# Optimization experiments

Hardware: AMD Instinct MI355X
Metric: run time of the kernel (lower is better)

## Reference

```python
import jax, jax.numpy as jnp
import numpy as np

N_NODES = 100000
N_EDGES = 3200000
IN_F, HID, N_CLS = 1433, 16, 7


def setup_inputs() -> dict:
    key = jax.random.key(0)
    ks = jax.random.split(key, 6)
    return {
        "x": jax.random.normal(ks[0], (N_NODES, IN_F), dtype=jnp.float32),
        "W1": jax.random.normal(ks[1], (IN_F, HID), dtype=jnp.float32) * 0.02,
        "b1": jax.random.normal(ks[2], (HID,), dtype=jnp.float32) * 0.02,
        "W2": jax.random.normal(ks[3], (HID, N_CLS), dtype=jnp.float32) * 0.1,
        "b2": jax.random.normal(ks[4], (N_CLS,), dtype=jnp.float32) * 0.1,
        "edge_index": jax.random.randint(ks[5], (2, N_EDGES), 0, N_NODES, dtype=jnp.int64),
    }


def _gcn_layer(h, W, b, row, col, n_nodes):
    # dense linear
    h = h @ W + b
    # symmetric degree normalization (self-loops already appended)
    deg = jax.ops.segment_sum(jnp.ones_like(col, dtype=h.dtype), col, num_segments=n_nodes)
    dinv = deg ** -0.5
    norm = dinv[row] * dinv[col]  # [E]
    # gather-scale-scatter message passing (aggr='add', source row -> target col)
    msgs = norm[:, None] * h[row]  # [E, F_out]
    return jax.ops.segment_sum(msgs, col, num_segments=n_nodes)


def reference(x, W1, b1, W2, b2, edge_index):
    n = x.shape[0]
    self_loops = jnp.broadcast_to(jnp.arange(n, dtype=edge_index.dtype)[None, :], (2, n))
    ei = jnp.concatenate([edge_index, self_loops], axis=1)
    row, col = ei[0], ei[1]
    h = jax.nn.relu(_gcn_layer(x, W1, b1, row, col, n))
    h = jax.nn.relu(_gcn_layer(h, W2, b2, row, col, n))
    return jax.nn.log_softmax(h, axis=1)
```

## Files before the change

### kernel.cpp

```cpp
#include <hip/hip_runtime.h>
#include <math.h>

constexpr int K_IN  = 1433;
constexpr int HID   = 16;
constexpr int NCLS  = 7;
constexpr int BLK   = 256;
constexpr int NB    = 256;
constexpr int NBLKA = 1024;

__device__ inline float4 wave_reduce4(float4 v) {
#pragma unroll
  for (int off = 32; off > 0; off >>= 1) {
    v.x += __shfl_xor(v.x, off);
    v.y += __shfl_xor(v.y, off);
    v.z += __shfl_xor(v.z, off);
    v.w += __shfl_xor(v.w, off);
  }
  return v;
}

__device__ inline int block_excl_scan256(int v, int* wsum) {
  const int lane = threadIdx.x & 63, wid = threadIdx.x >> 6;
  int s = v;
#pragma unroll
  for (int off = 1; off < 64; off <<= 1) {
    int t = __shfl_up(s, off);
    if (lane >= off) s += t;
  }
  if (lane == 63) wsum[wid] = s;
  __syncthreads();
  int woff = 0;
#pragma unroll
  for (int k = 0; k < 4; ++k) woff += (k < wid) ? wsum[k] : 0;
  return woff + s - v;
}


__global__ __launch_bounds__(256) void k_histA(const int* __restrict__ col,
                                               int* __restrict__ gHist, int nE) {
  __shared__ int h[NB];
  h[threadIdx.x] = 0;
  __syncthreads();
  const int ch = (nE + NBLKA - 1) / NBLKA;
  const int e0 = blockIdx.x * ch;
  const int e1 = min(e0 + ch, nE);
  for (int e = e0 + threadIdx.x; e < e1; e += 256) atomicAdd(&h[col[e] >> 9], 1);
  __syncthreads();
  gHist[threadIdx.x * NBLKA + blockIdx.x] = h[threadIdx.x];
}

__global__ __launch_bounds__(256) void k_scanA(int* __restrict__ gHist,
                                               int* __restrict__ bTot) {
  __shared__ int wsum[4];
  const int b = blockIdx.x, t = threadIdx.x;
  int4* p = (int4*)(gHist + (size_t)b * NBLKA);
  int4 c = p[t];
  const int tsum = c.x + c.y + c.z + c.w;
  const int base = block_excl_scan256(tsum, wsum);
  int4 o; o.x = base; o.y = base + c.x; o.z = o.y + c.y; o.w = o.z + c.z;
  p[t] = o;
  if (t == 255) bTot[b] = base + tsum;
}

__global__ __launch_bounds__(256) void k_placeA(const int* __restrict__ row,
                                                const int* __restrict__ col,
                                                const int* __restrict__ gHist,
                                                const int* __restrict__ bTot,
                                                int* __restrict__ sorted, int nE) {
  __shared__ int cur[NB];
  __shared__ int wsum[4];
  const int t = threadIdx.x;
  const int excl = block_excl_scan256(bTot[t], wsum);
  cur[t] = excl + gHist[t * NBLKA + blockIdx.x];
  __syncthreads();
  const int ch = (nE + NBLKA - 1) / NBLKA;
  const int e0 = blockIdx.x * ch;
  const int e1 = min(e0 + ch, nE);
  for (int e = e0 + t; e < e1; e += 256) {
    const int c = col[e];
    const int p = atomicAdd(&cur[c >> 9], 1);
    sorted[p] = ((c & 511) << 17) | row[e];
  }
}

__global__ __launch_bounds__(256) void k_bucketB(const int* __restrict__ sorted,
                                                 const int* __restrict__ bTot,
                                                 int* __restrict__ cnt,
                                                 int* __restrict__ start,
                                                 float* __restrict__ dinv,
                                                 int* __restrict__ rows, int n) {
  __shared__ int h[512];
  __shared__ int ls[512];
  __shared__ int sBase[NB];
  __shared__ int wsum[4];
  const int b = blockIdx.x, t = threadIdx.x;
  const int lane = t & 63, wid = t >> 6;
  h[t] = 0; h[t + 256] = 0;
  sBase[t] = block_excl_scan256(bTot[t], wsum);
  __syncthreads();
  const int s0 = sBase[b];
  const int s1 = (b < 255) ? sBase[b + 1] : s0 + bTot[b];
  for (int e = s0 + t; e < s1; e += 256) atomicAdd(&h[(sorted[e] >> 17) & 511], 1);
  __syncthreads();
  const int c0 = h[2 * t], c1 = h[2 * t + 1];
  const int tsum = c0 + c1;
  int s = tsum;
#pragma unroll
  for (int off = 1; off < 64; off <<= 1) { int v = __shfl_up(s, off); if (lane >= off) s += v; }
  if (lane == 63) wsum[wid] = s;
  __syncthreads();
  int woff = 0;
#pragma unroll
  for (int k = 0; k < 4; ++k) woff += (k < wid) ? wsum[k] : 0;
  const int base = woff + s - tsum;
  ls[2 * t] = base;
  ls[2 * t + 1] = base + c0;
  const int gc0 = b * 512 + 2 * t;
  if (gc0 < n) {
    cnt[gc0] = c0; start[gc0] = s0 + base;
    dinv[gc0] = rsqrtf((float)(c0 + 1));
  }
  if (gc0 + 1 < n) {
    cnt[gc0 + 1] = c1; start[gc0 + 1] = s0 + base + c0;
    dinv[gc0 + 1] = rsqrtf((float)(c1 + 1));
  }
  __syncthreads();
  for (int e = s0 + t; e < s1; e += 256) {
    const int rc = sorted[e];
    const int p = atomicAdd(&ls[(rc >> 17) & 511], 1);
    rows[s0 + p] = rc & 0x1FFFF;
  }
}


__global__ __launch_bounds__(BLK) void k_gemm1(const float* __restrict__ x,
                                               const float* __restrict__ W1,
                                               const float* __restrict__ b1,
                                               const float* __restrict__ dinv,
                                               float* __restrict__ h1s, int n) {
  const int lane = threadIdx.x & 63;
  const int wave = threadIdx.x >> 6;
  const int r0 = blockIdx.x * 16 + wave * 4;
  bool vr[4];
  const float* xr[4];
#pragma unroll
  for (int j = 0; j < 4; ++j) {
    vr[j] = (r0 + j) < n;
    xr[j] = x + (size_t)(vr[j] ? r0 + j : 0) * K_IN;
  }
  float acc[4][HID] = {};

  constexpr int NSTEP = (K_IN + 63) / 64;
#pragma unroll 2
  for (int s = 0; s < NSTEP - 1; ++s) {
    const int k = s * 64 + lane;
    const float4* wp = (const float4*)(W1 + (size_t)k * HID);
    const float4 w0 = wp[0], w1 = wp[1], w2 = wp[2], w3 = wp[3];
    float xv[4];
#pragma unroll
    for (int j = 0; j < 4; ++j) xv[j] = vr[j] ? xr[j][k] : 0.0f;
#pragma unroll
    for (int j = 0; j < 4; ++j) {
      acc[j][0]  = fmaf(xv[j], w0.x, acc[j][0]);
      acc[j][1]  = fmaf(xv[j], w0.y, acc[j][1]);
      acc[j][2]  = fmaf(xv[j], w0.z, acc[j][2]);
      acc[j][3]  = fmaf(xv[j], w0.w, acc[j][3]);
      acc[j][4]  = fmaf(xv[j], w1.x, acc[j][4]);
      acc[j][5]  = fmaf(xv[j], w1.y, acc[j][5]);
      acc[j][6]  = fmaf(xv[j], w1.z, acc[j][6]);
      acc[j][7]  = fmaf(xv[j], w1.w, acc[j][7]);
      acc[j][8]  = fmaf(xv[j], w2.x, acc[j][8]);
      acc[j][9]  = fmaf(xv[j], w2.y, acc[j][9]);
      acc[j][10] = fmaf(xv[j], w2.z, acc[j][10]);
      acc[j][11] = fmaf(xv[j], w2.w, acc[j][11]);
      acc[j][12] = fmaf(xv[j], w3.x, acc[j][12]);
      acc[j][13] = fmaf(xv[j], w3.y, acc[j][13]);
      acc[j][14] = fmaf(xv[j], w3.z, acc[j][14]);
      acc[j][15] = fmaf(xv[j], w3.w, acc[j][15]);
    }
  }
  {
    const int k = (NSTEP - 1) * 64 + lane;
    if (k < K_IN) {
      const float4* wp = (const float4*)(W1 + (size_t)k * HID);
      const float4 ww[4] = {wp[0], wp[1], wp[2], wp[3]};
      float xv[4];
#pragma unroll
      for (int j = 0; j < 4; ++j) xv[j] = vr[j] ? xr[j][k] : 0.0f;
#pragma unroll
      for (int j = 0; j < 4; ++j)
#pragma unroll
        for (int f4 = 0; f4 < 4; ++f4) {
          acc[j][f4 * 4 + 0] = fmaf(xv[j], ww[f4].x, acc[j][f4 * 4 + 0]);
          acc[j][f4 * 4 + 1] = fmaf(xv[j], ww[f4].y, acc[j][f4 * 4 + 1]);
          acc[j][f4 * 4 + 2] = fmaf(xv[j], ww[f4].z, acc[j][f4 * 4 + 2]);
          acc[j][f4 * 4 + 3] = fmaf(xv[j], ww[f4].w, acc[j][f4 * 4 + 3]);
        }
    }
  }

  const float4* b14 = (const float4*)b1;
#pragma unroll
  for (int j = 0; j < 4; ++j) {
    float4 a[4];
#pragma unroll
    for (int f4 = 0; f4 < 4; ++f4)
      a[f4] = wave_reduce4(make_float4(acc[j][f4 * 4], acc[j][f4 * 4 + 1],
                                       acc[j][f4 * 4 + 2], acc[j][f4 * 4 + 3]));
    if (lane == 0 && vr[j]) {
      const int r = r0 + j;
      const float d = dinv[r];
      float4* o = (float4*)(h1s + (size_t)r * HID);
#pragma unroll
      for (int f4 = 0; f4 < 4; ++f4) {
        const float4 bb = b14[f4];
        o[f4] = make_float4(d * (a[f4].x + bb.x), d * (a[f4].y + bb.y),
                            d * (a[f4].z + bb.z), d * (a[f4].w + bb.w));
      }
    }
  }
}

__global__ __launch_bounds__(BLK) void k_gather1g2(const int* __restrict__ rows,
                                                   const int* __restrict__ start,
                                                   const int* __restrict__ cnt,
                                                   const float* __restrict__ dinv,
                                                   const float* __restrict__ h1s,
                                                   const float* __restrict__ W2,
                                                   const float* __restrict__ b2,
                                                   float* __restrict__ h2s, int n) {
  __shared__ float w2s[HID * NCLS];
  __shared__ float b2s[NCLS];
  if (threadIdx.x < HID * NCLS) w2s[threadIdx.x] = W2[threadIdx.x];
  if (threadIdx.x < NCLS) b2s[threadIdx.x] = b2[threadIdx.x];
  __syncthreads();
  const int node = blockIdx.x * 4 + (threadIdx.x >> 6);
  const int lane = threadIdx.x & 63;
  const int f = lane & 15;
  const int g = lane >> 4;
  if (node >= n) return;
  const float dc = dinv[node];
  float acc = (g == 0) ? h1s[(size_t)node * HID + f] : 0.0f;
  const int m = cnt[node];
  const int* bp = rows + start[node];
  int q = g;
  for (; q + 4 < m; q += 8) {
    const int r0 = bp[q], r1 = bp[q + 4];
    acc += h1s[(size_t)r0 * HID + f];
    acc += h1s[(size_t)r1 * HID + f];
  }
  if (q < m) acc += h1s[(size_t)bp[q] * HID + f];
  acc += __shfl_xor(acc, 16);
  acc += __shfl_xor(acc, 32);
  acc = fmaxf(dc * acc, 0.0f);
  float sj[NCLS];
#pragma unroll
  for (int j = 0; j < NCLS; ++j) sj[j] = acc * w2s[f * NCLS + j];
#pragma unroll
  for (int off = 1; off < 16; off <<= 1)
#pragma unroll
    for (int j = 0; j < NCLS; ++j) sj[j] += __shfl_xor(sj[j], off);
  if (g == 0 && f < NCLS) {
    float v = sj[0];
#pragma unroll
    for (int j = 1; j < NCLS; ++j) if (f == j) v = sj[j];
    h2s[(size_t)node * NCLS + f] = dc * (v + b2s[f]);
  }
}

__global__ __launch_bounds__(BLK) void k_gather2(const int* __restrict__ rows,
                                                 const int* __restrict__ start,
                                                 const int* __restrict__ cnt,
                                                 const float* __restrict__ dinv,
                                                 const float* __restrict__ h2s,
                                                 float* __restrict__ out, int n) {
  const int node = blockIdx.x * 4 + (threadIdx.x >> 6);
  const int lane = threadIdx.x & 63;
  const int f = lane & 7;
  const int g = lane >> 3;
  if (node >= n) return;
  const float dc = dinv[node];
  float acc = (g == 0) ? h2s[(size_t)node * NCLS + f] : 0.0f;
  const int m = cnt[node];
  const int* bp = rows + start[node];
  int q = g;
  for (; q + 8 < m; q += 16) {
    const int r0 = bp[q], r1 = bp[q + 8];
    acc += h2s[(size_t)r0 * NCLS + f];
    acc += h2s[(size_t)r1 * NCLS + f];
  }
  if (q < m) acc += h2s[(size_t)bp[q] * NCLS + f];
  acc += __shfl_xor(acc, 8);
  acc += __shfl_xor(acc, 16);
  acc += __shfl_xor(acc, 32);
  const bool act = f < NCLS;
  const float t = fmaxf(dc * acc, 0.0f);
  float tm = act ? t : -1e30f;
#pragma unroll
  for (int off = 1; off < 8; off <<= 1) tm = fmaxf(tm, __shfl_xor(tm, off, 8));
  float se = act ? __expf(t - tm) : 0.0f;
#pragma unroll
  for (int off = 1; off < 8; off <<= 1) se += __shfl_xor(se, off, 8);
  const float lse = tm + __logf(se);
  if (g == 0 && act) out[(size_t)node * NCLS + f] = t - lse;
}

extern "C" void kernel_launch(void* const* d_in, const int* in_sizes, int n_in,
                              void* d_out, int out_size, void* d_ws, size_t ws_size,
                              hipStream_t stream) {
  const float* x  = (const float*)d_in[0];
  const float* W1 = (const float*)d_in[1];
  const float* b1 = (const float*)d_in[2];
  const float* W2 = (const float*)d_in[3];
  const float* b2 = (const float*)d_in[4];
  const int*   ei = (const int*)d_in[5];

  const int n  = in_sizes[0] / K_IN;
  const int nE = in_sizes[5] / 2;
  const int* row = ei;
  const int* col = ei + nE;

  char* w = (char*)d_ws;
  size_t off = 0;
  auto alloc = [&](size_t elems) {
    void* p = w + off;
    off += ((elems * 4 + 15) & ~(size_t)15);
    return p;
  };
  int*   cnt    = (int*)alloc(n);
  int*   start  = (int*)alloc(n);
  float* dinv   = (float*)alloc(n);
  float* h1s    = (float*)alloc((size_t)n * HID);
  float* h2s    = (float*)alloc((size_t)n * NCLS + 16);
  int*   gHist  = (int*)alloc((size_t)NB * NBLKA);
  int*   bTot   = (int*)alloc(NB);
  int*   sorted = (int*)alloc(nE);
  int*   rows   = (int*)alloc(nE);

  const int gG1 = (n + 15) / 16;
  const int gWN = (n + 3) / 4;

  k_histA<<<NBLKA, 256, 0, stream>>>(col, gHist, nE);
  k_scanA<<<NB, 256, 0, stream>>>(gHist, bTot);
  k_placeA<<<NBLKA, 256, 0, stream>>>(row, col, gHist, bTot, sorted, nE);
  k_bucketB<<<NB, 256, 0, stream>>>(sorted, bTot, cnt, start, dinv, rows, n);

  k_gemm1<<<gG1, BLK, 0, stream>>>(x, W1, b1, dinv, h1s, n);
  k_gather1g2<<<gWN, BLK, 0, stream>>>(rows, start, cnt, dinv, h1s, W2, b2, h2s, n);

  k_gather2<<<gWN, BLK, 0, stream>>>(rows, start, cnt, dinv, h2s, (float*)d_out, n);
}
```

Baseline: 419.2 us.

## Overlap GEMM1 with edge-sorting kernels by splitting it across fused launches

The dense x@W1 GEMM no longer waits for the degree computation. It no longer scales by dinv and is split into three row segments. Each segment runs as extra blocks inside the histogram, placement and bucket kernels, so the memory-bound GEMM overlaps the sorting phases. The dinv scaling moves into the first gather, which now loads dinv for each source row. This adds random reads per edge, and the hardcoded segment sizes assume n=100000.

```diff
diff --git a/kernel.cpp b/kernel.cpp
--- a/kernel.cpp
+++ b/kernel.cpp
@@ -7,6 +7,9 @@
 constexpr int BLK   = 256;
 constexpr int NB    = 256;
 constexpr int NBLKA = 1024;
+constexpr int GSEG1 = 2083;
+constexpr int GSEG2 = 2083;
+constexpr int GSEG3 = 2084;
 
 __device__ inline float4 wave_reduce4(float4 v) {
 #pragma unroll
@@ -35,112 +38,14 @@
   return woff + s - v;
 }
 
-
-__global__ __launch_bounds__(256) void k_histA(const int* __restrict__ col,
-                                               int* __restrict__ gHist, int nE) {
-  __shared__ int h[NB];
-  h[threadIdx.x] = 0;
-  __syncthreads();
-  const int ch = (nE + NBLKA - 1) / NBLKA;
-  const int e0 = blockIdx.x * ch;
-  const int e1 = min(e0 + ch, nE);
-  for (int e = e0 + threadIdx.x; e < e1; e += 256) atomicAdd(&h[col[e] >> 9], 1);
-  __syncthreads();
-  gHist[threadIdx.x * NBLKA + blockIdx.x] = h[threadIdx.x];
-}
-
-__global__ __launch_bounds__(256) void k_scanA(int* __restrict__ gHist,
-                                               int* __restrict__ bTot) {
-  __shared__ int wsum[4];
-  const int b = blockIdx.x, t = threadIdx.x;
-  int4* p = (int4*)(gHist + (size_t)b * NBLKA);
-  int4 c = p[t];
-  const int tsum = c.x + c.y + c.z + c.w;
-  const int base = block_excl_scan256(tsum, wsum);
-  int4 o; o.x = base; o.y = base + c.x; o.z = o.y + c.y; o.w = o.z + c.z;
-  p[t] = o;
-  if (t == 255) bTot[b] = base + tsum;
-}
-
-__global__ __launch_bounds__(256) void k_placeA(const int* __restrict__ row,
-                                                const int* __restrict__ col,
-                                                const int* __restrict__ gHist,
-                                                const int* __restrict__ bTot,
-                                                int* __restrict__ sorted, int nE) {
-  __shared__ int cur[NB];
-  __shared__ int wsum[4];
-  const int t = threadIdx.x;
-  const int excl = block_excl_scan256(bTot[t], wsum);
-  cur[t] = excl + gHist[t * NBLKA + blockIdx.x];
-  __syncthreads();
-  const int ch = (nE + NBLKA - 1) / NBLKA;
-  const int e0 = blockIdx.x * ch;
-  const int e1 = min(e0 + ch, nE);
-  for (int e = e0 + t; e < e1; e += 256) {
-    const int c = col[e];
-    const int p = atomicAdd(&cur[c >> 9], 1);
-    sorted[p] = ((c & 511) << 17) | row[e];
-  }
-}
-
-__global__ __launch_bounds__(256) void k_bucketB(const int* __restrict__ sorted,
-                                                 const int* __restrict__ bTot,
-                                                 int* __restrict__ cnt,
-                                                 int* __restrict__ start,
-                                                 float* __restrict__ dinv,
-                                                 int* __restrict__ rows, int n) {
-  __shared__ int h[512];
-  __shared__ int ls[512];
-  __shared__ int sBase[NB];
-  __shared__ int wsum[4];
-  const int b = blockIdx.x, t = threadIdx.x;
-  const int lane = t & 63, wid = t >> 6;
-  h[t] = 0; h[t + 256] = 0;
-  sBase[t] = block_excl_scan256(bTot[t], wsum);
-  __syncthreads();
-  const int s0 = sBase[b];
-  const int s1 = (b < 255) ? sBase[b + 1] : s0 + bTot[b];
-  for (int e = s0 + t; e < s1; e += 256) atomicAdd(&h[(sorted[e] >> 17) & 511], 1);
-  __syncthreads();
-  const int c0 = h[2 * t], c1 = h[2 * t + 1];
-  const int tsum = c0 + c1;
-  int s = tsum;
-#pragma unroll
-  for (int off = 1; off < 64; off <<= 1) { int v = __shfl_up(s, off); if (lane >= off) s += v; }
-  if (lane == 63) wsum[wid] = s;
-  __syncthreads();
-  int woff = 0;
-#pragma unroll
-  for (int k = 0; k < 4; ++k) woff += (k < wid) ? wsum[k] : 0;
-  const int base = woff + s - tsum;
-  ls[2 * t] = base;
-  ls[2 * t + 1] = base + c0;
-  const int gc0 = b * 512 + 2 * t;
-  if (gc0 < n) {
-    cnt[gc0] = c0; start[gc0] = s0 + base;
-    dinv[gc0] = rsqrtf((float)(c0 + 1));
-  }
-  if (gc0 + 1 < n) {
-    cnt[gc0 + 1] = c1; start[gc0 + 1] = s0 + base + c0;
-    dinv[gc0 + 1] = rsqrtf((float)(c1 + 1));
-  }
-  __syncthreads();
-  for (int e = s0 + t; e < s1; e += 256) {
-    const int rc = sorted[e];
-    const int p = atomicAdd(&ls[(rc >> 17) & 511], 1);
-    rows[s0 + p] = rc & 0x1FFFF;
-  }
-}
-
-
-__global__ __launch_bounds__(BLK) void k_gemm1(const float* __restrict__ x,
-                                               const float* __restrict__ W1,
-                                               const float* __restrict__ b1,
-                                               const float* __restrict__ dinv,
-                                               float* __restrict__ h1s, int n) {
+__device__ __forceinline__ void gemm1_block(int gblk,
+                                            const float* __restrict__ x,
+                                            const float* __restrict__ W1,
+                                            const float* __restrict__ b1,
+                                            float* __restrict__ h1lin, int n) {
   const int lane = threadIdx.x & 63;
   const int wave = threadIdx.x >> 6;
-  const int r0 = blockIdx.x * 16 + wave * 4;
+  const int r0 = gblk * 16 + wave * 4;
   bool vr[4];
   const float* xr[4];
 #pragma unroll
@@ -209,15 +114,135 @@
                                        acc[j][f4 * 4 + 2], acc[j][f4 * 4 + 3]));
     if (lane == 0 && vr[j]) {
       const int r = r0 + j;
-      const float d = dinv[r];
-      float4* o = (float4*)(h1s + (size_t)r * HID);
+      float4* o = (float4*)(h1lin + (size_t)r * HID);
 #pragma unroll
       for (int f4 = 0; f4 < 4; ++f4) {
         const float4 bb = b14[f4];
-        o[f4] = make_float4(d * (a[f4].x + bb.x), d * (a[f4].y + bb.y),
-                            d * (a[f4].z + bb.z), d * (a[f4].w + bb.w));
+        o[f4] = make_float4(a[f4].x + bb.x, a[f4].y + bb.y,
+                            a[f4].z + bb.z, a[f4].w + bb.w);
       }
     }
+  }
+}
+
+__global__ __launch_bounds__(256) void k_fusedA(const int* __restrict__ col,
+                                                int* __restrict__ gHist, int nE,
+                                                const float* __restrict__ x,
+                                                const float* __restrict__ W1,
+                                                const float* __restrict__ b1,
+                                                float* __restrict__ h1lin, int n) {
+  __shared__ int h[NB];
+  if (blockIdx.x < NBLKA) {
+    const int b = blockIdx.x;
+    h[threadIdx.x] = 0;
+    __syncthreads();
+    const int ch = (nE + NBLKA - 1) / NBLKA;
+    const int e0 = b * ch;
+    const int e1 = min(e0 + ch, nE);
+    for (int e = e0 + threadIdx.x; e < e1; e += 256) atomicAdd(&h[col[e] >> 9], 1);
+    __syncthreads();
+    gHist[threadIdx.x * NBLKA + b] = h[threadIdx.x];
+  } else {
+    gemm1_block(blockIdx.x - NBLKA, x, W1, b1, h1lin, n);
+  }
+}
+
+__global__ __launch_bounds__(256) void k_scanA(int* __restrict__ gHist,
+                                               int* __restrict__ bTot) {
+  __shared__ int wsum[4];
+  const int b = blockIdx.x, t = threadIdx.x;
+  int4* p = (int4*)(gHist + (size_t)b * NBLKA);
+  int4 c = p[t];
+  const int tsum = c.x + c.y + c.z + c.w;
+  const int base = block_excl_scan256(tsum, wsum);
+  int4 o; o.x = base; o.y = base + c.x; o.z = o.y + c.y; o.w = o.z + c.z;
+  p[t] = o;
+  if (t == 255) bTot[b] = base + tsum;
+}
+
+__global__ __launch_bounds__(256) void k_fusedB(const int* __restrict__ row,
+                                                const int* __restrict__ col,
+                                                const int* __restrict__ gHist,
+                                                const int* __restrict__ bTot,
+                                                int* __restrict__ sorted, int nE,
+                                                const float* __restrict__ x,
+                                                const float* __restrict__ W1,
+                                                const float* __restrict__ b1,
+                                                float* __restrict__ h1lin, int n) {
+  __shared__ int cur[NB];
+  __shared__ int wsum[4];
+  if (blockIdx.x < NBLKA) {
+    const int t = threadIdx.x;
+    const int excl = block_excl_scan256(bTot[t], wsum);
+    cur[t] = excl + gHist[t * NBLKA + blockIdx.x];
+    __syncthreads();
+    const int ch = (nE + NBLKA - 1) / NBLKA;
+    const int e0 = blockIdx.x * ch;
+    const int e1 = min(e0 + ch, nE);
+    for (int e = e0 + t; e < e1; e += 256) {
+      const int c = col[e];
+      const int p = atomicAdd(&cur[c >> 9], 1);
+      sorted[p] = ((c & 511) << 17) | row[e];
+    }
+  } else {
+    gemm1_block(GSEG1 + blockIdx.x - NBLKA, x, W1, b1, h1lin, n);
+  }
+}
+
+__global__ __launch_bounds__(256) void k_fusedC(const int* __restrict__ sorted,
+                                                const int* __restrict__ bTot,
+                                                int* __restrict__ cnt,
+                                                int* __restrict__ start,
+                                                float* __restrict__ dinv,
+                                                int* __restrict__ rows,
+                                                const float* __restrict__ x,
+                                                const float* __restrict__ W1,
+                                                const float* __restrict__ b1,
+                                                float* __restrict__ h1lin, int n) {
+  __shared__ int h[512];
+  __shared__ int ls[512];
+  __shared__ int sBase[NB];
+  __shared__ int wsum[4];
+  if (blockIdx.x < NB) {
+    const int b = blockIdx.x, t = threadIdx.x;
+    const int lane = t & 63, wid = t >> 6;
+    h[t] = 0; h[t + 256] = 0;
+    sBase[t] = block_excl_scan256(bTot[t], wsum);
+    __syncthreads();
+    const int s0 = sBase[b];
+    const int s1 = (b < 255) ? sBase[b + 1] : s0 + bTot[b];
+    for (int e = s0 + t; e < s1; e += 256) atomicAdd(&h[(sorted[e] >> 17) & 511], 1);
+    __syncthreads();
+    const int c0 = h[2 * t], c1 = h[2 * t + 1];
+    const int tsum = c0 + c1;
+    int s = tsum;
+#pragma unroll
+    for (int off = 1; off < 64; off <<= 1) { int v = __shfl_up(s, off); if (lane >= off) s += v; }
+    if (lane == 63) wsum[wid] = s;
+    __syncthreads();
+    int woff = 0;
+#pragma unroll
+    for (int k = 0; k < 4; ++k) woff += (k < wid) ? wsum[k] : 0;
+    const int base = woff + s - tsum;
+    ls[2 * t] = base;
+    ls[2 * t + 1] = base + c0;
+    const int gc0 = b * 512 + 2 * t;
+    if (gc0 < n) {
+      cnt[gc0] = c0; start[gc0] = s0 + base;
+      dinv[gc0] = rsqrtf((float)(c0 + 1));
+    }
+    if (gc0 + 1 < n) {
+      cnt[gc0 + 1] = c1; start[gc0 + 1] = s0 + base + c0;
+      dinv[gc0 + 1] = rsqrtf((float)(c1 + 1));
+    }
+    __syncthreads();
+    for (int e = s0 + t; e < s1; e += 256) {
+      const int rc = sorted[e];
+      const int p = atomicAdd(&ls[(rc >> 17) & 511], 1);
+      rows[s0 + p] = rc & 0x1FFFF;
+    }
+  } else {
+    gemm1_block(GSEG1 + GSEG2 + blockIdx.x - NB, x, W1, b1, h1lin, n);
   }
 }
 
@@ -225,7 +250,7 @@
                                                    const int* __restrict__ start,
                                                    const int* __restrict__ cnt,
                                                    const float* __restrict__ dinv,
-                                                   const float* __restrict__ h1s,
+                                                   const float* __restrict__ h1lin,
                                                    const float* __restrict__ W2,
                                                    const float* __restrict__ b2,
                                                    float* __restrict__ h2s, int n) {
@@ -240,16 +265,19 @@
   const int g = lane >> 4;
   if (node >= n) return;
   const float dc = dinv[node];
-  float acc = (g == 0) ? h1s[(size_t)node * HID + f] : 0.0f;
+  float acc = (g == 0) ? dc * h1lin[(size_t)node * HID + f] : 0.0f;
   const int m = cnt[node];
   const int* bp = rows + start[node];
   int q = g;
   for (; q + 4 < m; q += 8) {
     const int r0 = bp[q], r1 = bp[q + 4];
-    acc += h1s[(size_t)r0 * HID + f];
-    acc += h1s[(size_t)r1 * HID + f];
-  }
-  if (q < m) acc += h1s[(size_t)bp[q] * HID + f];
+    acc = fmaf(dinv[r0], h1lin[(size_t)r0 * HID + f], acc);
+    acc = fmaf(dinv[r1], h1lin[(size_t)r1 * HID + f], acc);
+  }
+  if (q < m) {
+    const int r0 = bp[q];
+    acc = fmaf(dinv[r0], h1lin[(size_t)r0 * HID + f], acc);
+  }
   acc += __shfl_xor(acc, 16);
   acc += __shfl_xor(acc, 32);
   acc = fmaxf(dc * acc, 0.0f);
@@ -330,23 +358,22 @@
   int*   cnt    = (int*)alloc(n);
   int*   start  = (int*)alloc(n);
   float* dinv   = (float*)alloc(n);
-  float* h1s    = (float*)alloc((size_t)n * HID);
+  float* h1lin  = (float*)alloc((size_t)n * HID);
   float* h2s    = (float*)alloc((size_t)n * NCLS + 16);
   int*   gHist  = (int*)alloc((size_t)NB * NBLKA);
   int*   bTot   = (int*)alloc(NB);
   int*   sorted = (int*)alloc(nE);
   int*   rows   = (int*)alloc(nE);
 
-  const int gG1 = (n + 15) / 16;
   const int gWN = (n + 3) / 4;
 
-  k_histA<<<NBLKA, 256, 0, stream>>>(col, gHist, nE);
+  k_fusedA<<<NBLKA + GSEG1, 256, 0, stream>>>(col, gHist, nE, x, W1, b1, h1lin, n);
   k_scanA<<<NB, 256, 0, stream>>>(gHist, bTot);
-  k_placeA<<<NBLKA, 256, 0, stream>>>(row, col, gHist, bTot, sorted, nE);
-  k_bucketB<<<NB, 256, 0, stream>>>(sorted, bTot, cnt, start, dinv, rows, n);
-
-  k_gemm1<<<gG1, BLK, 0, stream>>>(x, W1, b1, dinv, h1s, n);
-  k_gather1g2<<<gWN, BLK, 0, stream>>>(rows, start, cnt, dinv, h1s, W2, b2, h2s, n);
-
+  k_fusedB<<<NBLKA + GSEG2, 256, 0, stream>>>(row, col, gHist, bTot, sorted, nE,
+                                              x, W1, b1, h1lin, n);
+  k_fusedC<<<NB + GSEG3, 256, 0, stream>>>(sorted, bTot, cnt, start, dinv, rows,
+                                           x, W1, b1, h1lin, n);
+
+  k_gather1g2<<<gWN, BLK, 0, stream>>>(rows, start, cnt, dinv, h1lin, W2, b2, h2s, n);
   k_gather2<<<gWN, BLK, 0, stream>>>(rows, start, cnt, dinv, h2s, (float*)d_out, n);
 }
```

Measured after the change: 439.1 us. 4.8% more time.
